# Performance work log

Hardware: AMD Instinct MI355X
Metric: run time of the kernel (lower is better)

The kernel has to match this reference:

```python
import jax, jax.numpy as jnp
import numpy as np

B, T, I, H, D, C, OUT = 32, 128, 64, 256, 32, 64, 32
DECAY = 0.99

def _lin(k, fi, fo):
    lim = 1.0 / np.sqrt(fi)
    kw, kb = jax.random.split(k)
    W = jax.random.uniform(kw, (fi, fo), minval=-lim, maxval=lim, dtype=jnp.float32)
    b = jax.random.uniform(kb, (fo,), minval=-lim, maxval=lim, dtype=jnp.float32)
    return W, b

def setup_inputs():
    key = jax.random.key(0)
    ks = jax.random.split(key, 12)
    x = jax.random.normal(ks[0], (B, T, I), dtype=jnp.float32)
    lengths = jax.random.randint(ks[1], (B,), 1, T + 1)
    W_dg1, b_dg1 = _lin(ks[2], I + H, D)
    W_dg2, b_dg2 = _lin(ks[3], D, D)
    W_e1, b_e1 = _lin(ks[4], 2 * I, H)
    W_e2, b_e2 = _lin(ks[5], H, H)
    W_ih, b_ih = _lin(ks[6], H, 3 * H)
    W_hh, b_hh = _lin(ks[7], H, 3 * H)
    W_f1, b_f1 = _lin(ks[8], H, H)
    W_f2, b_f2 = _lin(ks[9], H, C)
    return dict(x=x, lengths=lengths, out_lengths=OUT,
                W_dg1=W_dg1, b_dg1=b_dg1, W_dg2=W_dg2, b_dg2=b_dg2,
                W_e1=W_e1, b_e1=b_e1, W_e2=W_e2, b_e2=b_e2,
                W_ih=W_ih, b_ih=b_ih, W_hh=W_hh, b_hh=b_hh,
                W_f1=W_f1, b_f1=b_f1, W_f2=W_f2, b_f2=b_f2)

def _forward(x, lengths, out_lengths, W_dg1, b_dg1, W_dg2, b_dg2, W_e1, b_e1, W_e2, b_e2,
             W_ih, b_ih, W_hh, b_hh, W_f1, b_f1, W_f2, b_f2):
    Bs, Ts, Is = x.shape
    Ds = W_dg2.shape[1]
    Hs = W_e2.shape[1]
    decay = DECAY ** jnp.arange(1, Ds + 1, dtype=x.dtype)  # [D]
    d_idx = jnp.arange(Ds)
    gkey = jax.random.key(42)
    g_enc = jax.random.gumbel(jax.random.fold_in(gkey, 0), (Ts, Bs, Ds), x.dtype)
    g_dec = jax.random.gumbel(jax.random.fold_in(gkey, 1), (out_lengths, Bs, Ds), x.dtype)
    masks = (jnp.arange(Ts)[None, :] < lengths[:, None]).astype(x.dtype)  # [B,T]

    def gumbel_softmax_hard(logits, g):
        # F.gumbel_softmax(..., tau=1.0, hard=True) straight-through estimator
        y_soft = jax.nn.softmax(logits + g, axis=-1)
        y_hard = jax.nn.one_hot(jnp.argmax(y_soft, axis=-1), Ds, dtype=logits.dtype)
        return y_hard + y_soft - jax.lax.stop_gradient(y_soft)

    def gru_cell(xin, h):
        # torch.nn.GRUCell gate order: r, z, n
        gi = xin @ W_ih + b_ih
        gh = h @ W_hh + b_hh
        i_r, i_z, i_n = jnp.split(gi, 3, axis=-1)
        h_r, h_z, h_n = jnp.split(gh, 3, axis=-1)
        r = jax.nn.sigmoid(i_r + h_r)
        z = jax.nn.sigmoid(i_z + h_z)
        n = jnp.tanh(i_n + r * h_n)
        return (1.0 - z) * n + z * h

    def step_core(buf, h, x_t, g_t, mem_t):
        cell_in = jnp.concatenate([x_t, h], axis=-1)
        logits = jax.nn.elu(cell_in @ W_dg1 + b_dg1) @ W_dg2 + b_dg2
        gate = gumbel_softmax_hard(logits, g_t)  # [B,D]
        # shift buffer along dim 1 (new[:, :-1] = old[:, 1:], last slot zeroed)
        new_buf = jnp.concatenate([buf[:, 1:], jnp.zeros_like(buf[:, :1])], axis=1)
        upd = x_t[:, None, :] * decay[None, :, None] * gate[:, :, None]  # [B,D,I]
        new_buf = new_buf.at[:, d_idx, d_idx].set(upd)  # diagonal scatter-assign
        rnn_in = jnp.concatenate([x_t, mem_t], axis=-1)
        rnn_in = jax.nn.elu(rnn_in @ W_e1 + b_e1) @ W_e2 + b_e2
        return new_buf, gru_cell(rnn_in, h)

    buf0 = jnp.zeros((Bs, Ds + 1, Ds, Is), x.dtype)
    h0 = jnp.zeros((Bs, Hs), x.dtype)

    def enc_step(carry, inp):
        buf, h = carry
        x_t, m_t, g_t = inp
        mem_t = buf[:, 0].sum(axis=1)  # [B,I]
        buf, nh = step_core(buf, h, x_t, g_t, mem_t)
        h = m_t[:, None] * nh + (1.0 - m_t[:, None]) * h
        return (buf, h), None

    (buf, h), _ = jax.lax.scan(enc_step, (buf0, h0),
                               (jnp.swapaxes(x, 0, 1), masks.T, g_enc))

    x_zero = jnp.zeros((Bs, Is), x.dtype)

    def dec_step(carry, g_t):
        buf, h = carry
        # get_current_memory(slide=True): roll -1 along dim1 with last slot zeroed
        buf = jnp.concatenate([buf[:, 1:], jnp.zeros_like(buf[:, :1])], axis=1)
        mem_t = buf[:, 0].sum(axis=1)
        buf, nh = step_core(buf, h, x_zero, g_t, mem_t)
        out = jax.nn.relu(nh @ W_f1 + b_f1) @ W_f2 + b_f2
        return (buf, nh), out

    _, outs = jax.lax.scan(dec_step, (buf, h), g_dec)  # [OUT,B,C]
    return jnp.swapaxes(outs, 0, 1)  # [B,OUT,C]

def reference(x, lengths, out_lengths, W_dg1, b_dg1, W_dg2, b_dg2, W_e1, b_e1, W_e2, b_e2,
              W_ih, b_ih, W_hh, b_hh, W_f1, b_f1, W_f2, b_f2):
    return _forward(x, lengths, out_lengths, W_dg1, b_dg1, W_dg2, b_dg2, W_e1, b_e1,
                    W_e2, b_e2, W_ih, b_ih, W_hh, b_hh, W_f1, b_f1, W_f2, b_f2)
```

## Files before the change

kernel.cpp:

```cpp
#include <hip/hip_runtime.h>
#include <math.h>


#define kB 32
#define kT 128
#define kI 64
#define kH 256
#define kD 32
#define kC 64
#define kOut 32
#define kSteps (kT + kOut)
#define NB 89
#define NTHR 256
#define NT_ALL (NB * NTHR)

#define WS_FL    384
#define WS_H     1856
#define WS_SEL   (WS_H + 4*8192)
#define WS_MEM   (WS_SEL + 128)
#define WS_NZ    (WS_MEM + kB*kSteps*kI)
#define WS_LIN   WS_NZ
#define WS_O1    (WS_LIN + 4*8192)
#define WS_W2    (WS_O1 + 4*8192)
#define WS_B2    (WS_W2 + kH*3*kH)
#define WS_G     (WS_B2 + 3*kH)
#define WS_P     (WS_G + kT*kB*kD)
#define WS_ZERO_BYTES ((size_t)WS_NZ * sizeof(float))

__device__ __forceinline__ float cload(const float* p) {
  return __hip_atomic_load(p, __ATOMIC_RELAXED, __HIP_MEMORY_SCOPE_AGENT);
}
__device__ __forceinline__ void cstore(float* p, float v) {
  __hip_atomic_store(p, v, __ATOMIC_RELAXED, __HIP_MEMORY_SCOPE_AGENT);
}
__device__ __forceinline__ int cload_i(const int* p) {
  return __hip_atomic_load(p, __ATOMIC_RELAXED, __HIP_MEMORY_SCOPE_AGENT);
}
__device__ __forceinline__ void cstore_i(int* p, int v) {
  __hip_atomic_store(p, v, __ATOMIC_RELAXED, __HIP_MEMORY_SCOPE_AGENT);
}
__device__ __forceinline__ float4 cload4(const float* p) {
  float4 r;
  asm volatile("global_load_dwordx4 %0, %1, off sc0 sc1" : "=v"(r) : "v"(p));
  return r;
}
__device__ __forceinline__ void waitvm() {
  asm volatile("s_waitcnt vmcnt(0)" ::: "memory");
}

__device__ __forceinline__ void poll(const int* FL, int tid,
                                     int tH, int tDG, int tE, int tF1, int tF2) {
  int thr;
  if      (tid < 32) thr = tH;
  else if (tid == 32) thr = tDG;
  else if (tid < 65) thr = tE;
  else if (tid < 81) thr = tF1;
  else if (tid < 89) thr = tF2;
  else thr = 0;
  const int* p = FL + tid * 16;
  for (;;) {
    int ok = (thr <= 0) || (cload_i(p) >= thr);
    if (__syncthreads_count(ok) == NTHR) return;
    __builtin_amdgcn_s_sleep(2);
  }
}
__device__ __forceinline__ void setflag(int* FL, int tid, int idx, int val) {
  waitvm();
  __syncthreads();
  if (tid == 0) cstore_i(FL + idx * 16, val);
}

__device__ __forceinline__ void tf2x32(unsigned k0, unsigned k1,
                                       unsigned x0, unsigned x1,
                                       unsigned& o0, unsigned& o1) {
  unsigned ks2 = k0 ^ k1 ^ 0x1BD11BDAu;
  unsigned v0 = x0 + k0, v1 = x1 + k1;
#define TFR(r) { v0 += v1; v1 = (v1 << (r)) | (v1 >> (32-(r))); v1 ^= v0; }
  TFR(13) TFR(15) TFR(26) TFR(6)   v0 += k1;  v1 += ks2 + 1u;
  TFR(17) TFR(29) TFR(16) TFR(24)  v0 += ks2; v1 += k0  + 2u;
  TFR(13) TFR(15) TFR(26) TFR(6)   v0 += k0;  v1 += k1  + 3u;
  TFR(17) TFR(29) TFR(16) TFR(24)  v0 += k1;  v1 += ks2 + 4u;
  TFR(13) TFR(15) TFR(26) TFR(6)   v0 += ks2; v1 += k0  + 5u;
#undef TFR
  o0 = v0; o1 = v1;
}
__device__ __forceinline__ float bits_to_gumbel(unsigned bits) {
  float f = __uint_as_float((bits >> 9) | 0x3F800000u) - 1.0f;
  float u = f + 1.17549435e-38f;
  return -logf(-logf(u));
}

__device__ __forceinline__ void gridbar_full(unsigned* u, unsigned target) {
  __syncthreads();
  if (threadIdx.x == 0) {
    __threadfence();
    __hip_atomic_fetch_add(&u[320], 1u, __ATOMIC_ACQ_REL, __HIP_MEMORY_SCOPE_AGENT);
    while (__hip_atomic_load(&u[320], __ATOMIC_RELAXED, __HIP_MEMORY_SCOPE_AGENT) < target)
      __builtin_amdgcn_s_sleep(1);
    __threadfence();
  }
  __syncthreads();
}

__device__ __forceinline__ float elu1(float v) { return v > 0.f ? v : expm1f(v); }

__global__ __launch_bounds__(NTHR)
void delay_rnn(const float* __restrict__ x, const int* __restrict__ lengths,
               const float* __restrict__ W_dg1, const float* __restrict__ b_dg1,
               const float* __restrict__ W_dg2, const float* __restrict__ b_dg2,
               const float* __restrict__ W_e1,  const float* __restrict__ b_e1,
               const float* __restrict__ W_e2,  const float* __restrict__ b_e2,
               const float* __restrict__ W_ih,  const float* __restrict__ b_ih,
               const float* __restrict__ W_hh,  const float* __restrict__ b_hh,
               const float* __restrict__ W_f1,  const float* __restrict__ b_f1,
               const float* __restrict__ W_f2,  const float* __restrict__ b_f2,
               float* __restrict__ out, float* __restrict__ ws) {
  const int tid = threadIdx.x;
  const int bid = blockIdx.x;
  const int gid = bid * NTHR + tid;

  unsigned* baru = (unsigned*)ws;
  int*   FL    = (int*)(ws + WS_FL);
  float* hBuf  = ws + WS_H;
  int*   selG  = (int*)(ws + WS_SEL);
  float* mem   = ws + WS_MEM;
  float* linB  = ws + WS_LIN;
  float* o1B   = ws + WS_O1;
  float* W2g   = ws + WS_W2;
  float* B2g   = ws + WS_B2;
  float* g     = ws + WS_G;
  float* Pg    = ws + WS_P;

  __shared__ float S[35264];
  __shared__ float lgarr[1056];
  __shared__ float sb1[32], sb2[32], dec_sh[32];
  __shared__ int   sel[32], len_s[32];

  {
    unsigned k0, k1;
    tf2x32(0u, 42u, 0u, 0u, k0, k1);
    for (int i = gid; i < kT * kB * kD; i += NT_ALL) {
      unsigned a, b;
      tf2x32(k0, k1, 0u, (unsigned)i, a, b);
      g[i] = bits_to_gumbel(a ^ b);
    }
  }
  for (int idx = gid; idx < kH * 3 * kH; idx += NT_ALL) {
    int k = idx / (3 * kH), n = idx % (3 * kH);
    const float* wr = W_e2 + k * kH;
    float s0 = 0, s1 = 0, s2 = 0, s3 = 0;
    for (int m = 0; m < kH; m += 4) {
      float4 wv = *(const float4*)(wr + m);
      s0 += wv.x * W_ih[(m    ) * 3 * kH + n];
      s1 += wv.y * W_ih[(m + 1) * 3 * kH + n];
      s2 += wv.z * W_ih[(m + 2) * 3 * kH + n];
      s3 += wv.w * W_ih[(m + 3) * 3 * kH + n];
    }
    W2g[idx] = ((s0 + s1) + (s2 + s3));
  }
  for (int n = gid; n < 3 * kH; n += NT_ALL) {
    float s = b_ih[n];
    for (int m = 0; m < kH; ++m) s += b_e2[m] * W_ih[m * 3 * kH + n];
    B2g[n] = s;
  }
  for (int idx = gid; idx < kT * kB * kH; idx += NT_ALL) {
    int s = idx >> 13, r = idx & 8191, b = r >> 8, j = r & 255;
    const float* xr = x + (b * kT + s) * kI;
    float a0 = 0, a1 = 0, a2 = 0, a3 = 0;
    for (int k = 0; k < 64; k += 4) {
      float4 xv = *(const float4*)(xr + k);
      a0 += xv.x * W_e1[(64 + k) * 256 + j];
      a1 += xv.y * W_e1[(65 + k) * 256 + j];
      a2 += xv.z * W_e1[(66 + k) * 256 + j];
      a3 += xv.w * W_e1[(67 + k) * 256 + j];
    }
    Pg[idx] = ((a0 + a1) + (a2 + a3));
  }

  gridbar_full(baru, NB);

  if (bid < 32) {
    float* whh = S; float* w2 = S + 6240;
    const int jb = bid * 8;
    for (int i = tid; i < 6144; i += NTHR) {
      int gg = i >> 11, r = i & 2047, jj = r >> 8, k = r & 255;
      whh[(gg * 8 + jj) * 260 + k] = W_hh[k * 768 + gg * 256 + jb + jj];
      w2 [(gg * 8 + jj) * 260 + k] = W2g [k * 768 + gg * 256 + jb + jj];
    }
    if (tid < 24) { int gg = tid / 8, jj = tid % 8;
      sb1[tid] = b_hh[gg * 256 + jb + jj];
      sb2[tid] = B2g [gg * 256 + jb + jj];
    }
    if (tid < 32) len_s[tid] = lengths[tid];
    __syncthreads();

    float* sH = S + 12480; float* sLin = S + 20800;
    float* red = S + 29120;
    for (int s = 0; s < kSteps; ++s) {
      int tDG = (s >= 1) ? (s < kT ? s : kT) : 0;
      int tF1 = (s >= kT + 4) ? (s - 2) : 0;
      poll(FL, tid, s, tDG, s + 1, tF1, 0);

      const float* hR = hBuf + (s & 3) * 8192;
      const float* lR = linB + (s & 3) * 8192;
      const bool useC = (s >= 1 && s < kT);
      const float4* P4 = (const float4*)(Pg + (s - 1) * 8192);
      const int* selR = selG + ((s - 1) & 3) * 32;
      float4 th[8], tl[8], tp[8];
      int tsel[8];
      #pragma unroll
      for (int u8 = 0; u8 < 8; ++u8) {
        int i4 = (tid + u8 * 256) * 4;
        th[u8] = cload4(hR + i4);
        tl[u8] = cload4(lR + i4);
      }
      if (useC) {
        #pragma unroll
        for (int u8 = 0; u8 < 8; ++u8) {
          int idx = tid + u8 * 256; int b = idx >> 6, k4 = idx & 63;
          tp[u8] = P4[b * 64 + k4];
          tsel[u8] = cload_i(&selR[b]);
        }
      }
      waitvm();
      #pragma unroll
      for (int u8 = 0; u8 < 8; ++u8) {
        int idx = tid + u8 * 256; int b = idx >> 6, k4 = idx & 63;
        *(float4*)&sH[b * 260 + k4 * 4] = th[u8];
        float cx = 0.f, cy = 0.f, cz = 0.f, cw = 0.f;
        if (useC && tsel[u8] == 0) {
          cx = 0.99f * tp[u8].x; cy = 0.99f * tp[u8].y;
          cz = 0.99f * tp[u8].z; cw = 0.99f * tp[u8].w;
        }
        float4 v;
        v.x = elu1(tl[u8].x + cx);
        v.y = elu1(tl[u8].y + cy);
        v.z = elu1(tl[u8].z + cz);
        v.w = elu1(tl[u8].w + cw);
        *(float4*)&sLin[b * 260 + k4 * 4] = v;
      }
      __syncthreads();
      const float4* sH4 = (const float4*)sH;
      const float4* sL4 = (const float4*)sLin;
      const float4* wh4 = (const float4*)whh;
      const float4* w24 = (const float4*)w2;
      const int c  = tid & 7;
      const int b4 = (tid >> 3) & 7;
      const int kq = tid >> 6;
      float acc[24];
      #pragma unroll
      for (int a = 0; a < 24; ++a) acc[a] = 0.f;
      for (int kk = 0; kk < 16; ++kk) {
        int k4 = kq * 16 + kk;
        float4 wr[6];
        #pragma unroll
        for (int gg = 0; gg < 3; ++gg) {
          wr[gg]     = wh4[(gg * 8 + c) * 65 + k4];
          wr[3 + gg] = w24[(gg * 8 + c) * 65 + k4];
        }
        #pragma unroll
        for (int bi = 0; bi < 4; ++bi) {
          int b = bi * 8 + b4;
          float4 h4 = sH4[b * 65 + k4];
          float4 l4 = sL4[b * 65 + k4];
          #pragma unroll
          for (int gg = 0; gg < 3; ++gg) {
            float4 w = wr[gg];
            acc[bi * 6 + gg]     += h4.x * w.x + h4.y * w.y + h4.z * w.z + h4.w * w.w;
            w = wr[3 + gg];
            acc[bi * 6 + 3 + gg] += l4.x * w.x + l4.y * w.y + l4.z * w.z + l4.w * w.w;
          }
        }
      }
      #pragma unroll
      for (int bi = 0; bi < 4; ++bi)
        #pragma unroll
        for (int rr = 0; rr < 6; ++rr)
          red[kq * 1536 + rr * 256 + (bi * 8 + b4) * 8 + c] = acc[bi * 6 + rr];
      __syncthreads();
      {
        int b = tid >> 3, cc = tid & 7, jg = bid * 8 + cc;
        int lo = b * 8 + cc;
        float dots[6];
        #pragma unroll
        for (int rr = 0; rr < 6; ++rr)
          dots[rr] = (red[rr * 256 + lo] + red[1536 + rr * 256 + lo]) +
                     (red[3072 + rr * 256 + lo] + red[4608 + rr * 256 + lo]);
        float ghr = dots[0] + sb1[cc];
        float ghz = dots[1] + sb1[8 + cc];
        float ghn = dots[2] + sb1[16 + cc];
        float gir = dots[3] + sb2[cc];
        float giz = dots[4] + sb2[8 + cc];
        float gin = dots[5] + sb2[16 + cc];
        float r = 1.f / (1.f + expf(-(gir + ghr)));
        float z = 1.f / (1.f + expf(-(giz + ghz)));
        float n = tanhf(gin + r * ghn);
        float hold = sH[b * 260 + jg];
        float nh = (1.f - z) * n + z * hold;
        float hv = (s < kT) ? ((s < len_s[b]) ? nh : hold) : nh;
        cstore(&hBuf[((s + 1) & 3) * 8192 + b * 256 + jg], hv);
      }
      setflag(FL, tid, bid, s + 1);
    }
  }
  else if (bid < 64) {
    float* we1 = S;
    const int jb = (bid - 32) * 8;
    for (int i = tid; i < 1024; i += NTHR) {
      int jj = i >> 7, k = i & 127;
      we1[jj * 132 + k] = W_e1[k * 256 + jb + jj];
    }
    if (tid < 8) sb1[tid] = b_e1[jb + tid];
    __syncthreads();

    float* sx = S + 1056; float* sm = S + 3232;
    for (int e = 0; e < kSteps; ++e) {
      int tDG = e - 1 < 0 ? 0 : (e - 1 > kT ? kT : e - 1);
      poll(FL, tid, e - 2, tDG, 0, 0, 0);

      const bool encx = (e < kT);
      float4 tm[2];
      #pragma unroll
      for (int u2 = 0; u2 < 2; ++u2) {
        int idx = tid + u2 * 256; int b = idx >> 4, k4 = idx & 15;
        tm[u2] = cload4(mem + (b * kSteps + e) * kI + k4 * 4);
      }
      waitvm();
      #pragma unroll
      for (int u2 = 0; u2 < 2; ++u2) {
        int idx = tid + u2 * 256; int b = idx >> 4, k4 = idx & 15;
        *(float4*)&sm[b * 68 + k4 * 4] = tm[u2];
        if (encx)
          *(float4*)&sx[b * 68 + k4 * 4] =
              *(const float4*)(x + (b * kT + e) * kI + k4 * 4);
      }
      __syncthreads();
      const int b = tid >> 3, jj = tid & 7;
      const float4* sx4 = (const float4*)sx;
      const float4* sm4 = (const float4*)sm;
      const float4* w4p = (const float4*)we1;
      float a0 = 0, a1 = 0, a2 = 0, a3 = 0;
      if (encx) {
        for (int k4 = 0; k4 < 16; ++k4) {
          float4 xv = sx4[b * 17 + k4], w = w4p[jj * 33 + k4];
          a0 += xv.x * w.x; a1 += xv.y * w.y; a2 += xv.z * w.z; a3 += xv.w * w.w;
        }
      }
      for (int k4 = 0; k4 < 16; ++k4) {
        float4 mv = sm4[b * 17 + k4], w = w4p[jj * 33 + 16 + k4];
        a0 += mv.x * w.x; a1 += mv.y * w.y; a2 += mv.z * w.z; a3 += mv.w * w.w;
      }
      cstore(&linB[(e & 3) * 8192 + b * 256 + jb + jj],
             ((a0 + a1) + (a2 + a3)) + sb1[jj]);
      __syncthreads();
      setflag(FL, tid, 33 + (bid - 32), e + 1);
    }
  }
  else if (bid < 80) {
    float* wf1 = S;
    const int jb = (bid - 64) * 16;
    for (int i = tid; i < 4096; i += NTHR) {
      int jj = i >> 8, k = i & 255;
      wf1[jj * 260 + k] = W_f1[k * 256 + jb + jj];
    }
    if (tid < 16) sb1[tid] = b_f1[jb + tid];
    __syncthreads();

    float* sHf = S + 4160; float* red = S + 12480;
    for (int s = kT + 1; s <= kSteps; ++s) {
      int tF2 = (s >= kT + 5) ? (s - 2) : 0;
      poll(FL, tid, s, 0, 0, 0, tF2);

      const float* hR = hBuf + (s & 3) * 8192;
      float4 th[8];
      #pragma unroll
      for (int u8 = 0; u8 < 8; ++u8) th[u8] = cload4(hR + (tid + u8 * 256) * 4);
      waitvm();
      #pragma unroll
      for (int u8 = 0; u8 < 8; ++u8) {
        int idx = tid + u8 * 256; int b = idx >> 6, k4 = idx & 63;
        *(float4*)&sHf[b * 260 + k4 * 4] = th[u8];
      }
      __syncthreads();
      const float4* sH4 = (const float4*)sHf;
      const float4* w4p = (const float4*)wf1;
      const int cq = tid & 3, b4 = (tid >> 2) & 7, kq = tid >> 5;
      float acc[16];
      #pragma unroll
      for (int a = 0; a < 16; ++a) acc[a] = 0.f;
      for (int kk = 0; kk < 8; ++kk) {
        int k4 = kq * 8 + kk;
        float4 wr[4];
        #pragma unroll
        for (int ci = 0; ci < 4; ++ci) wr[ci] = w4p[(cq * 4 + ci) * 65 + k4];
        #pragma unroll
        for (int bi = 0; bi < 4; ++bi) {
          float4 h4 = sH4[(bi * 8 + b4) * 65 + k4];
          #pragma unroll
          for (int ci = 0; ci < 4; ++ci) {
            float4 w = wr[ci];
            acc[bi * 4 + ci] += h4.x * w.x + h4.y * w.y + h4.z * w.z + h4.w * w.w;
          }
        }
      }
      #pragma unroll
      for (int bi = 0; bi < 4; ++bi)
        #pragma unroll
        for (int ci = 0; ci < 4; ++ci)
          red[kq * 512 + (bi * 4 + ci) * 32 + cq * 8 + b4] = acc[bi * 4 + ci];
      __syncthreads();
      #pragma unroll
      for (int u2 = 0; u2 < 2; ++u2) {
        int o = tid * 2 + u2; int b = o >> 4, col = o & 15;
        int gg = ((b >> 3) * 4 + (col & 3)) * 32 + (col >> 2) * 8 + (b & 7);
        float v = 0.f;
        #pragma unroll
        for (int kq2 = 0; kq2 < 8; ++kq2) v += red[kq2 * 512 + gg];
        v += sb1[col];
        cstore(&o1B[(s & 3) * 8192 + b * 256 + (bid - 64) * 16 + col],
               v > 0.f ? v : 0.f);
      }
      __syncthreads();
      setflag(FL, tid, 65 + (bid - 64), s + 1);
    }
  }
  else if (bid < 88) {
    float* wf2 = S;
    const int cb = (bid - 80) * 8;
    for (int i = tid; i < 2048; i += NTHR) {
      int cc = i >> 8, k = i & 255;
      wf2[cc * 260 + k] = W_f2[k * 64 + cb + cc];
    }
    if (tid < 8) sb2[tid] = b_f2[cb + tid];
    __syncthreads();

    float* sO = S + 2080; float* red = S + 10400;
    for (int s = kT + 2; s <= kSteps + 1; ++s) {
      poll(FL, tid, 0, 0, 0, s, 0);

      const float* oR = o1B + ((s - 1) & 3) * 8192;
      float4 to[8];
      #pragma unroll
      for (int u8 = 0; u8 < 8; ++u8) to[u8] = cload4(oR + (tid + u8 * 256) * 4);
      waitvm();
      #pragma unroll
      for (int u8 = 0; u8 < 8; ++u8) {
        int idx = tid + u8 * 256; int b = idx >> 6, k4 = idx & 63;
        *(float4*)&sO[b * 260 + k4 * 4] = to[u8];
      }
      __syncthreads();
      const float4* sO4 = (const float4*)sO;
      const float4* w4p = (const float4*)wf2;
      const int c = tid & 7, b4 = (tid >> 3) & 7, kq = tid >> 6;
      float acc[4] = {0.f, 0.f, 0.f, 0.f};
      for (int kk = 0; kk < 16; ++kk) {
        int k4 = kq * 16 + kk;
        float4 w = w4p[c * 65 + k4];
        #pragma unroll
        for (int bi = 0; bi < 4; ++bi) {
          float4 o4 = sO4[(bi * 8 + b4) * 65 + k4];
          acc[bi] += o4.x * w.x + o4.y * w.y + o4.z * w.z + o4.w * w.w;
        }
      }
      #pragma unroll
      for (int bi = 0; bi < 4; ++bi)
        red[kq * 256 + bi * 64 + b4 * 8 + c] = acc[bi];
      __syncthreads();
      { int b = tid >> 3, col = tid & 7;
        int gg = (b >> 3) * 64 + (b & 7) * 8 + col;
        float v = (red[gg] + red[256 + gg]) + (red[512 + gg] + red[768 + gg]);
        out[(b * kOut + (s - 2 - kT)) * kC + (bid - 80) * 8 + col] =
            v + sb2[col];
      }
      __syncthreads();
      setflag(FL, tid, 81 + (bid - 80), s + 1);
    }
  }
  else {
    float* wdg1 = S; float* wdg2 = S + 10368;
    for (int i = tid; i < 10240; i += NTHR) {
      int j = i / 320, k = i % 320;
      wdg1[j * 324 + k] = W_dg1[k * 32 + j];
    }
    for (int i = tid; i < 1024; i += NTHR) wdg2[i] = W_dg2[i];
    if (tid < 32) { sb1[tid] = b_dg1[tid]; sb2[tid] = b_dg2[tid];
                    dec_sh[tid] = powf(0.99f, (float)(tid + 1)); }
    __syncthreads();

    float* sXH = S + 11392;
    float* red = S + 21760;
    float* l1s = S + 25856;
    for (int s = 0; s < kT; ++s) {
      poll(FL, tid, s, 0, 0, 0, 0);

      const float* hR = hBuf + (s & 3) * 8192;
      float4 th[8];
      #pragma unroll
      for (int u8 = 0; u8 < 8; ++u8) th[u8] = cload4(hR + (tid + u8 * 256) * 4);
      waitvm();
      #pragma unroll
      for (int u8 = 0; u8 < 8; ++u8) {
        int idx = tid + u8 * 256; int b = idx >> 6, k4 = idx & 63;
        *(float4*)&sXH[b * 324 + 64 + k4 * 4] = th[u8];
      }
      #pragma unroll
      for (int u2 = 0; u2 < 2; ++u2) {
        int idx = tid + u2 * 256; int b = idx >> 4, k4 = idx & 15;
        *(float4*)&sXH[b * 324 + k4 * 4] =
            *(const float4*)(x + (b * kT + s) * kI + k4 * 4);
      }
      __syncthreads();
      {
        const float4* sA4 = (const float4*)sXH;
        const float4* wd4 = (const float4*)wdg1;
        const int cq = tid & 7, b4 = (tid >> 3) & 7, kq = tid >> 6;
        float acc[16];
        #pragma unroll
        for (int a = 0; a < 16; ++a) acc[a] = 0.f;
        for (int kk = 0; kk < 20; ++kk) {
          int k4 = kq * 20 + kk;
          float4 wr[4];
          #pragma unroll
          for (int ci = 0; ci < 4; ++ci) wr[ci] = wd4[(cq * 4 + ci) * 81 + k4];
          #pragma unroll
          for (int bi = 0; bi < 4; ++bi) {
            float4 a4 = sA4[(bi * 8 + b4) * 81 + k4];
            #pragma unroll
            for (int ci = 0; ci < 4; ++ci) {
              float4 w = wr[ci];
              acc[bi * 4 + ci] += a4.x * w.x + a4.y * w.y + a4.z * w.z + a4.w * w.w;
            }
          }
        }
        #pragma unroll
        for (int bi = 0; bi < 4; ++bi)
          #pragma unroll
          for (int ci = 0; ci < 4; ++ci)
            red[kq * 1024 + (ci * 4 + bi) * 64 + cq * 8 + b4] = acc[bi * 4 + ci];
        __syncthreads();
        #pragma unroll
        for (int u4 = 0; u4 < 4; ++u4) {
          int o = tid * 4 + u4; int b = o >> 5, col = o & 31;
          int ci = col & 3, cq2 = col >> 2, bi = b >> 3, b42 = b & 7;
          int f = (ci * 4 + bi) * 64 + cq2 * 8 + b42;
          float v = (red[f] + red[1024 + f]) + (red[2048 + f] + red[3072 + f]);
          l1s[b * 36 + col] = elu1(v + sb1[col]);
        }
      }
      __syncthreads();
      for (int it = 0; it < 4; ++it) {
        int i = tid + it * 256; int b = i >> 5, j = i & 31;
        float sv = sb2[j];
        for (int k = 0; k < 32; ++k) sv += l1s[b * 36 + k] * wdg2[k * 32 + j];
        lgarr[b * 33 + j] = sv + g[(s * 32 + b) * 32 + j];
      }
      __syncthreads();
      if (tid < 32) {
        float best = lgarr[tid * 33]; int bi = 0;
        for (int j = 1; j < 32; ++j) {
          float v = lgarr[tid * 33 + j];
          if (v > best) { best = v; bi = j; }
        }
        sel[tid] = bi;
      }
      __syncthreads();
      if (tid < 32) cstore_i(&selG[(s & 3) * 32 + tid], sel[tid]);
      for (int it = 0; it < 8; ++it) {
        int i = tid + it * 256; int b = i >> 6, ii = i & 63;
        int d = sel[b];
        if (d > 0) {
          int c = s + 1 + d, e = -1;
          if (c < kT) e = c;
          else { int rr = c - kT - 1;
                 if (rr >= 0 && !(rr & 1)) { int kk = rr >> 1; if (kk < kOut) e = kT + kk; } }
          if (e >= 0) {
            float* p = &mem[(b * kSteps + e) * kI + ii];
            cstore(p, cload(p) + sXH[b * 324 + ii] * dec_sh[d]);
          }
        }
      }
      setflag(FL, tid, 32, s + 1);
    }
  }
}

extern "C" void kernel_launch(void* const* d_in, const int* in_sizes, int n_in,
                              void* d_out, int out_size, void* d_ws, size_t ws_size,
                              hipStream_t stream) {
  (void)in_sizes; (void)n_in; (void)out_size; (void)ws_size;
  const float* x      = (const float*)d_in[0];
  const int*   lens   = (const int*)  d_in[1];
  const float* W_dg1  = (const float*)d_in[3];
  const float* b_dg1  = (const float*)d_in[4];
  const float* W_dg2  = (const float*)d_in[5];
  const float* b_dg2  = (const float*)d_in[6];
  const float* W_e1   = (const float*)d_in[7];
  const float* b_e1   = (const float*)d_in[8];
  const float* W_e2   = (const float*)d_in[9];
  const float* b_e2   = (const float*)d_in[10];
  const float* W_ih   = (const float*)d_in[11];
  const float* b_ih   = (const float*)d_in[12];
  const float* W_hh   = (const float*)d_in[13];
  const float* b_hh   = (const float*)d_in[14];
  const float* W_f1   = (const float*)d_in[15];
  const float* b_f1   = (const float*)d_in[16];
  const float* W_f2   = (const float*)d_in[17];
  const float* b_f2   = (const float*)d_in[18];

  hipMemsetAsync(d_ws, 0, WS_ZERO_BYTES, stream);
  delay_rnn<<<dim3(NB), dim3(NTHR), 0, stream>>>(
      x, lens, W_dg1, b_dg1, W_dg2, b_dg2, W_e1, b_e1, W_e2, b_e2,
      W_ih, b_ih, W_hh, b_hh, W_f1, b_f1, W_f2, b_f2,
      (float*)d_out, (float*)d_ws);
}
```

Baseline: 1.941 ms.

## Fold encoder-linear and delay-gate blocks into GRU blocks, precompute input projection

Removes the dedicated encoder-linear blocks and the single delay-gate block. The x-part of the first encoder linear is now precomputed for all steps in the prologue. Each GRU block redundantly computes the delay-gate argmax itself and applies the delayed memory contribution straight into the precomputed linear buffer, using the already projected P rows. This cuts the grid from 89 to 56 blocks and removes two inter-block flag hops on the recurrent critical path. In exchange, every GRU block repeats the small gate matmul each step, and the prologue grows.

```diff
diff --git a/kernel.cpp b/kernel.cpp
--- a/kernel.cpp
+++ b/kernel.cpp
@@ -10,21 +10,20 @@
 #define kC 64
 #define kOut 32
 #define kSteps (kT + kOut)
-#define NB 89
+#define NB 56
 #define NTHR 256
 #define NT_ALL (NB * NTHR)
 
 #define WS_FL    384
 #define WS_H     1856
-#define WS_SEL   (WS_H + 4*8192)
-#define WS_MEM   (WS_SEL + 128)
-#define WS_NZ    (WS_MEM + kB*kSteps*kI)
-#define WS_LIN   WS_NZ
-#define WS_O1    (WS_LIN + 4*8192)
-#define WS_W2    (WS_O1 + 4*8192)
+#define WS_NZ    (WS_H + 4*8192)
+#define WS_DG1T  WS_NZ
+#define WS_W2    (WS_DG1T + 32*320)
 #define WS_B2    (WS_W2 + kH*3*kH)
 #define WS_G     (WS_B2 + 3*kH)
 #define WS_P     (WS_G + kT*kB*kD)
+#define WS_LINF  (WS_P + kT*kB*kH)
+#define WS_O1    (WS_LINF + kSteps*kB*kH)
 #define WS_ZERO_BYTES ((size_t)WS_NZ * sizeof(float))
 
 __device__ __forceinline__ float cload(const float* p) {
@@ -44,18 +43,21 @@
   asm volatile("global_load_dwordx4 %0, %1, off sc0 sc1" : "=v"(r) : "v"(p));
   return r;
 }
+__device__ __forceinline__ void cstore4(float* p, float4 v) {
+  cstore(p + 0, v.x); cstore(p + 1, v.y);
+  cstore(p + 2, v.z); cstore(p + 3, v.w);
+}
 __device__ __forceinline__ void waitvm() {
   asm volatile("s_waitcnt vmcnt(0)" ::: "memory");
 }
 
 __device__ __forceinline__ void poll(const int* FL, int tid,
-                                     int tH, int tDG, int tE, int tF1, int tF2) {
+                                     int tH, int tD, int tF1, int tF2) {
   int thr;
   if      (tid < 32) thr = tH;
-  else if (tid == 32) thr = tDG;
-  else if (tid < 65) thr = tE;
-  else if (tid < 81) thr = tF1;
-  else if (tid < 89) thr = tF2;
+  else if (tid < 64) thr = tD;
+  else if (tid < 80) thr = tF1;
+  else if (tid < 88) thr = tF2;
   else thr = 0;
   const int* p = FL + tid * 16;
   for (;;) {
@@ -122,19 +124,17 @@
   unsigned* baru = (unsigned*)ws;
   int*   FL    = (int*)(ws + WS_FL);
   float* hBuf  = ws + WS_H;
-  int*   selG  = (int*)(ws + WS_SEL);
-  float* mem   = ws + WS_MEM;
-  float* linB  = ws + WS_LIN;
-  float* o1B   = ws + WS_O1;
+  float* dg1T  = ws + WS_DG1T;
   float* W2g   = ws + WS_W2;
   float* B2g   = ws + WS_B2;
   float* g     = ws + WS_G;
   float* Pg    = ws + WS_P;
-
-  __shared__ float S[35264];
-  __shared__ float lgarr[1056];
-  __shared__ float sb1[32], sb2[32], dec_sh[32];
-  __shared__ int   sel[32], len_s[32];
+  float* linF  = ws + WS_LINF;
+  float* o1B   = ws + WS_O1;
+
+  __shared__ float S[38464];
+  __shared__ float sb1[32], sb2[32], dec_sh[32], dgb1[32], dgb2[32];
+  __shared__ int   sel_sh[32], len_s[32];
 
   {
     unsigned k0, k1;
@@ -144,6 +144,10 @@
       tf2x32(k0, k1, 0u, (unsigned)i, a, b);
       g[i] = bits_to_gumbel(a ^ b);
     }
+  }
+  for (int i = gid; i < 32 * 320; i += NT_ALL) {
+    int j = i / 320, k = i % 320;
+    dg1T[i] = W_dg1[k * 32 + j];
   }
   for (int idx = gid; idx < kH * 3 * kH; idx += NT_ALL) {
     int k = idx / (3 * kH), n = idx % (3 * kH);
@@ -176,61 +180,76 @@
     }
     Pg[idx] = ((a0 + a1) + (a2 + a3));
   }
+  for (int idx = gid; idx < kSteps * kB * kH; idx += NT_ALL) {
+    int e = idx >> 13, r = idx & 8191, b = r >> 8, j = r & 255;
+    float v = b_e1[j];
+    if (e < kT) {
+      const float* xr = x + (b * kT + e) * kI;
+      float a0 = 0, a1 = 0, a2 = 0, a3 = 0;
+      for (int k = 0; k < 64; k += 4) {
+        float4 xv = *(const float4*)(xr + k);
+        a0 += xv.x * W_e1[(k    ) * 256 + j];
+        a1 += xv.y * W_e1[(k + 1) * 256 + j];
+        a2 += xv.z * W_e1[(k + 2) * 256 + j];
+        a3 += xv.w * W_e1[(k + 3) * 256 + j];
+      }
+      v += ((a0 + a1) + (a2 + a3));
+    }
+    linF[idx] = v;
+  }
 
   gridbar_full(baru, NB);
 
   if (bid < 32) {
     float* whh = S; float* w2 = S + 6240;
+    float* sH = S + 12480; float* sLin = S + 20800;
+    float* red = S + 29120;
+    float* sX = S + 35264;
+    float* wdg2 = S + 37440;
     const int jb = bid * 8;
     for (int i = tid; i < 6144; i += NTHR) {
       int gg = i >> 11, r = i & 2047, jj = r >> 8, k = r & 255;
       whh[(gg * 8 + jj) * 260 + k] = W_hh[k * 768 + gg * 256 + jb + jj];
       w2 [(gg * 8 + jj) * 260 + k] = W2g [k * 768 + gg * 256 + jb + jj];
     }
+    for (int i = tid; i < 1024; i += NTHR) wdg2[i] = W_dg2[i];
     if (tid < 24) { int gg = tid / 8, jj = tid % 8;
       sb1[tid] = b_hh[gg * 256 + jb + jj];
       sb2[tid] = B2g [gg * 256 + jb + jj];
     }
-    if (tid < 32) len_s[tid] = lengths[tid];
+    if (tid < 32) {
+      len_s[tid] = lengths[tid];
+      dgb1[tid] = b_dg1[tid]; dgb2[tid] = b_dg2[tid];
+      dec_sh[tid] = powf(0.99f, (float)(tid + 1));
+    }
     __syncthreads();
 
-    float* sH = S + 12480; float* sLin = S + 20800;
-    float* red = S + 29120;
     for (int s = 0; s < kSteps; ++s) {
-      int tDG = (s >= 1) ? (s < kT ? s : kT) : 0;
+      int tD  = (s >= 2) ? ((s < kT) ? (s - 1) : kT) : 0;
       int tF1 = (s >= kT + 4) ? (s - 2) : 0;
-      poll(FL, tid, s, tDG, s + 1, tF1, 0);
+      poll(FL, tid, s, tD, tF1, 0);
 
       const float* hR = hBuf + (s & 3) * 8192;
-      const float* lR = linB + (s & 3) * 8192;
+      const float* lR = linF + s * 8192;
       const bool useC = (s >= 1 && s < kT);
       const float4* P4 = (const float4*)(Pg + (s - 1) * 8192);
-      const int* selR = selG + ((s - 1) & 3) * 32;
-      float4 th[8], tl[8], tp[8];
-      int tsel[8];
+      float4 th[8], tl[8];
       #pragma unroll
       for (int u8 = 0; u8 < 8; ++u8) {
         int i4 = (tid + u8 * 256) * 4;
         th[u8] = cload4(hR + i4);
         tl[u8] = cload4(lR + i4);
       }
-      if (useC) {
-        #pragma unroll
-        for (int u8 = 0; u8 < 8; ++u8) {
-          int idx = tid + u8 * 256; int b = idx >> 6, k4 = idx & 63;
-          tp[u8] = P4[b * 64 + k4];
-          tsel[u8] = cload_i(&selR[b]);
-        }
-      }
       waitvm();
       #pragma unroll
       for (int u8 = 0; u8 < 8; ++u8) {
         int idx = tid + u8 * 256; int b = idx >> 6, k4 = idx & 63;
         *(float4*)&sH[b * 260 + k4 * 4] = th[u8];
         float cx = 0.f, cy = 0.f, cz = 0.f, cw = 0.f;
-        if (useC && tsel[u8] == 0) {
-          cx = 0.99f * tp[u8].x; cy = 0.99f * tp[u8].y;
-          cz = 0.99f * tp[u8].z; cw = 0.99f * tp[u8].w;
+        if (useC && sel_sh[b] == 0) {
+          float4 p = P4[b * 64 + k4];
+          cx = 0.99f * p.x; cy = 0.99f * p.y;
+          cz = 0.99f * p.z; cw = 0.99f * p.w;
         }
         float4 v;
         v.x = elu1(tl[u8].x + cx);
@@ -301,64 +320,102 @@
         cstore(&hBuf[((s + 1) & 3) * 8192 + b * 256 + jg], hv);
       }
       setflag(FL, tid, bid, s + 1);
-    }
-  }
-  else if (bid < 64) {
-    float* we1 = S;
-    const int jb = (bid - 32) * 8;
-    for (int i = tid; i < 1024; i += NTHR) {
-      int jj = i >> 7, k = i & 127;
-      we1[jj * 132 + k] = W_e1[k * 256 + jb + jj];
-    }
-    if (tid < 8) sb1[tid] = b_e1[jb + tid];
-    __syncthreads();
-
-    float* sx = S + 1056; float* sm = S + 3232;
-    for (int e = 0; e < kSteps; ++e) {
-      int tDG = e - 1 < 0 ? 0 : (e - 1 > kT ? kT : e - 1);
-      poll(FL, tid, e - 2, tDG, 0, 0, 0);
-
-      const bool encx = (e < kT);
-      float4 tm[2];
-      #pragma unroll
-      for (int u2 = 0; u2 < 2; ++u2) {
-        int idx = tid + u2 * 256; int b = idx >> 4, k4 = idx & 15;
-        tm[u2] = cload4(mem + (b * kSteps + e) * kI + k4 * 4);
-      }
-      waitvm();
-      #pragma unroll
-      for (int u2 = 0; u2 < 2; ++u2) {
-        int idx = tid + u2 * 256; int b = idx >> 4, k4 = idx & 15;
-        *(float4*)&sm[b * 68 + k4 * 4] = tm[u2];
-        if (encx)
-          *(float4*)&sx[b * 68 + k4 * 4] =
-              *(const float4*)(x + (b * kT + e) * kI + k4 * 4);
-      }
-      __syncthreads();
-      const int b = tid >> 3, jj = tid & 7;
-      const float4* sx4 = (const float4*)sx;
-      const float4* sm4 = (const float4*)sm;
-      const float4* w4p = (const float4*)we1;
-      float a0 = 0, a1 = 0, a2 = 0, a3 = 0;
-      if (encx) {
-        for (int k4 = 0; k4 < 16; ++k4) {
-          float4 xv = sx4[b * 17 + k4], w = w4p[jj * 33 + k4];
-          a0 += xv.x * w.x; a1 += xv.y * w.y; a2 += xv.z * w.z; a3 += xv.w * w.w;
-        }
-      }
-      for (int k4 = 0; k4 < 16; ++k4) {
-        float4 mv = sm4[b * 17 + k4], w = w4p[jj * 33 + 16 + k4];
-        a0 += mv.x * w.x; a1 += mv.y * w.y; a2 += mv.z * w.z; a3 += mv.w * w.w;
-      }
-      cstore(&linB[(e & 3) * 8192 + b * 256 + jb + jj],
-             ((a0 + a1) + (a2 + a3)) + sb1[jj]);
-      __syncthreads();
-      setflag(FL, tid, 33 + (bid - 32), e + 1);
-    }
-  }
-  else if (bid < 80) {
+
+      if (s < kT) {
+        #pragma unroll
+        for (int u2 = 0; u2 < 2; ++u2) {
+          int idx = tid + u2 * 256; int b = idx >> 4, k4 = idx & 15;
+          *(float4*)&sX[b * 68 + k4 * 4] =
+              *(const float4*)(x + (b * kT + s) * kI + k4 * 4);
+        }
+        __syncthreads();
+        {
+          const float4* sX4 = (const float4*)sX;
+          const float4* sHq = (const float4*)sH;
+          const float4* wd4 = (const float4*)dg1T;
+          const int cq = tid & 7, b42 = (tid >> 3) & 7, kq2 = tid >> 6;
+          float acc2[16];
+          #pragma unroll
+          for (int a = 0; a < 16; ++a) acc2[a] = 0.f;
+          for (int kk = 0; kk < 20; ++kk) {
+            int k4 = kq2 * 20 + kk;
+            float4 wr[4];
+            #pragma unroll
+            for (int ci = 0; ci < 4; ++ci) wr[ci] = wd4[(cq * 4 + ci) * 80 + k4];
+            const bool isx = (k4 < 16);
+            #pragma unroll
+            for (int bi = 0; bi < 4; ++bi) {
+              int b = bi * 8 + b42;
+              float4 a4 = isx ? sX4[b * 17 + k4] : sHq[b * 65 + (k4 - 16)];
+              #pragma unroll
+              for (int ci = 0; ci < 4; ++ci) {
+                float4 w = wr[ci];
+                acc2[bi * 4 + ci] += a4.x * w.x + a4.y * w.y + a4.z * w.z + a4.w * w.w;
+              }
+            }
+          }
+          #pragma unroll
+          for (int bi = 0; bi < 4; ++bi)
+            #pragma unroll
+            for (int ci = 0; ci < 4; ++ci)
+              red[kq2 * 1024 + (ci * 4 + bi) * 64 + cq * 8 + b42] = acc2[bi * 4 + ci];
+        }
+        __syncthreads();
+        float* l1s = red + 4096;
+        #pragma unroll
+        for (int u4 = 0; u4 < 4; ++u4) {
+          int o = tid * 4 + u4; int b = o >> 5, col = o & 31;
+          int ci = col & 3, cq2 = col >> 2, bi = b >> 3, b42 = b & 7;
+          int f = (ci * 4 + bi) * 64 + cq2 * 8 + b42;
+          float v = (red[f] + red[1024 + f]) + (red[2048 + f] + red[3072 + f]);
+          l1s[b * 36 + col] = elu1(v + dgb1[col]);
+        }
+        __syncthreads();
+        float* lg = red;
+        for (int it = 0; it < 4; ++it) {
+          int i = tid + it * 256; int b = i >> 5, j = i & 31;
+          float sv = dgb2[j];
+          for (int k = 0; k < 32; ++k) sv += l1s[b * 36 + k] * wdg2[k * 32 + j];
+          lg[b * 33 + j] = sv + g[(s * 32 + b) * 32 + j];
+        }
+        __syncthreads();
+        if (tid < 32) {
+          float best = lg[tid * 33]; int bj = 0;
+          for (int j = 1; j < 32; ++j) {
+            float v = lg[tid * 33 + j];
+            if (v > best) { best = v; bj = j; }
+          }
+          sel_sh[tid] = bj;
+        }
+        __syncthreads();
+        {
+          int d = sel_sh[bid];
+          if (d > 0) {
+            int cc = s + 1 + d, e = -1;
+            if (cc < kT) e = cc;
+            else { int rr = cc - kT - 1;
+                   if (rr >= 0 && !(rr & 1)) {
+                     int kk2 = rr >> 1; if (kk2 < kOut) e = kT + kk2; } }
+            if (e >= 0 && tid < 64) {
+              float dec = dec_sh[d];
+              float* rowp = linF + e * 8192 + bid * 256;
+              const float* Prow = Pg + s * 8192 + bid * 256;
+              float4 v = cload4(rowp + tid * 4);
+              float4 p = *(const float4*)(Prow + tid * 4);
+              waitvm();
+              v.x += dec * p.x; v.y += dec * p.y;
+              v.z += dec * p.z; v.w += dec * p.w;
+              cstore4(rowp + tid * 4, v);
+            }
+          }
+        }
+        setflag(FL, tid, 32 + bid, s + 1);
+      }
+    }
+  }
+  else if (bid < 48) {
     float* wf1 = S;
-    const int jb = (bid - 64) * 16;
+    const int jb = (bid - 32) * 16;
     for (int i = tid; i < 4096; i += NTHR) {
       int jj = i >> 8, k = i & 255;
       wf1[jj * 260 + k] = W_f1[k * 256 + jb + jj];
@@ -369,7 +426,7 @@
     float* sHf = S + 4160; float* red = S + 12480;
     for (int s = kT + 1; s <= kSteps; ++s) {
       int tF2 = (s >= kT + 5) ? (s - 2) : 0;
-      poll(FL, tid, s, 0, 0, 0, tF2);
+      poll(FL, tid, s, 0, 0, tF2);
 
       const float* hR = hBuf + (s & 3) * 8192;
       float4 th[8];
@@ -417,16 +474,16 @@
         #pragma unroll
         for (int kq2 = 0; kq2 < 8; ++kq2) v += red[kq2 * 512 + gg];
         v += sb1[col];
-        cstore(&o1B[(s & 3) * 8192 + b * 256 + (bid - 64) * 16 + col],
+        cstore(&o1B[(s & 3) * 8192 + b * 256 + (bid - 32) * 16 + col],
                v > 0.f ? v : 0.f);
       }
       __syncthreads();
-      setflag(FL, tid, 65 + (bid - 64), s + 1);
-    }
-  }
-  else if (bid < 88) {
+      setflag(FL, tid, 64 + (bid - 32), s + 1);
+    }
+  }
+  else {
     float* wf2 = S;
-    const int cb = (bid - 80) * 8;
+    const int cb = (bid - 48) * 8;
     for (int i = tid; i < 2048; i += NTHR) {
       int cc = i >> 8, k = i & 255;
       wf2[cc * 260 + k] = W_f2[k * 64 + cb + cc];
@@ -436,7 +493,7 @@
 
     float* sO = S + 2080; float* red = S + 10400;
     for (int s = kT + 2; s <= kSteps + 1; ++s) {
-      poll(FL, tid, 0, 0, 0, s, 0);
+      poll(FL, tid, 0, 0, s, 0);
 
       const float* oR = o1B + ((s - 1) & 3) * 8192;
       float4 to[8];
@@ -469,117 +526,11 @@
       { int b = tid >> 3, col = tid & 7;
         int gg = (b >> 3) * 64 + (b & 7) * 8 + col;
         float v = (red[gg] + red[256 + gg]) + (red[512 + gg] + red[768 + gg]);
-        out[(b * kOut + (s - 2 - kT)) * kC + (bid - 80) * 8 + col] =
+        out[(b * kOut + (s - 2 - kT)) * kC + (bid - 48) * 8 + col] =
             v + sb2[col];
       }
       __syncthreads();
-      setflag(FL, tid, 81 + (bid - 80), s + 1);
-    }
-  }
-  else {
-    float* wdg1 = S; float* wdg2 = S + 10368;
-    for (int i = tid; i < 10240; i += NTHR) {
-      int j = i / 320, k = i % 320;
-      wdg1[j * 324 + k] = W_dg1[k * 32 + j];
-    }
-    for (int i = tid; i < 1024; i += NTHR) wdg2[i] = W_dg2[i];
-    if (tid < 32) { sb1[tid] = b_dg1[tid]; sb2[tid] = b_dg2[tid];
-                    dec_sh[tid] = powf(0.99f, (float)(tid + 1)); }
-    __syncthreads();
-
-    float* sXH = S + 11392;
-    float* red = S + 21760;
-    float* l1s = S + 25856;
-    for (int s = 0; s < kT; ++s) {
-      poll(FL, tid, s, 0, 0, 0, 0);
-
-      const float* hR = hBuf + (s & 3) * 8192;
-      float4 th[8];
-      #pragma unroll
-      for (int u8 = 0; u8 < 8; ++u8) th[u8] = cload4(hR + (tid + u8 * 256) * 4);
-      waitvm();
-      #pragma unroll
-      for (int u8 = 0; u8 < 8; ++u8) {
-        int idx = tid + u8 * 256; int b = idx >> 6, k4 = idx & 63;
-        *(float4*)&sXH[b * 324 + 64 + k4 * 4] = th[u8];
-      }
-      #pragma unroll
-      for (int u2 = 0; u2 < 2; ++u2) {
-        int idx = tid + u2 * 256; int b = idx >> 4, k4 = idx & 15;
-        *(float4*)&sXH[b * 324 + k4 * 4] =
-            *(const float4*)(x + (b * kT + s) * kI + k4 * 4);
-      }
-      __syncthreads();
-      {
-        const float4* sA4 = (const float4*)sXH;
-        const float4* wd4 = (const float4*)wdg1;
-        const int cq = tid & 7, b4 = (tid >> 3) & 7, kq = tid >> 6;
-        float acc[16];
-        #pragma unroll
-        for (int a = 0; a < 16; ++a) acc[a] = 0.f;
-        for (int kk = 0; kk < 20; ++kk) {
-          int k4 = kq * 20 + kk;
-          float4 wr[4];
-          #pragma unroll
-          for (int ci = 0; ci < 4; ++ci) wr[ci] = wd4[(cq * 4 + ci) * 81 + k4];
-          #pragma unroll
-          for (int bi = 0; bi < 4; ++bi) {
-            float4 a4 = sA4[(bi * 8 + b4) * 81 + k4];
-            #pragma unroll
-            for (int ci = 0; ci < 4; ++ci) {
-              float4 w = wr[ci];
-              acc[bi * 4 + ci] += a4.x * w.x + a4.y * w.y + a4.z * w.z + a4.w * w.w;
-            }
-          }
-        }
-        #pragma unroll
-        for (int bi = 0; bi < 4; ++bi)
-          #pragma unroll
-          for (int ci = 0; ci < 4; ++ci)
-            red[kq * 1024 + (ci * 4 + bi) * 64 + cq * 8 + b4] = acc[bi * 4 + ci];
-        __syncthreads();
-        #pragma unroll
-        for (int u4 = 0; u4 < 4; ++u4) {
-          int o = tid * 4 + u4; int b = o >> 5, col = o & 31;
-          int ci = col & 3, cq2 = col >> 2, bi = b >> 3, b42 = b & 7;
-          int f = (ci * 4 + bi) * 64 + cq2 * 8 + b42;
-          float v = (red[f] + red[1024 + f]) + (red[2048 + f] + red[3072 + f]);
-          l1s[b * 36 + col] = elu1(v + sb1[col]);
-        }
-      }
-      __syncthreads();
-      for (int it = 0; it < 4; ++it) {
-        int i = tid + it * 256; int b = i >> 5, j = i & 31;
-        float sv = sb2[j];
-        for (int k = 0; k < 32; ++k) sv += l1s[b * 36 + k] * wdg2[k * 32 + j];
-        lgarr[b * 33 + j] = sv + g[(s * 32 + b) * 32 + j];
-      }
-      __syncthreads();
-      if (tid < 32) {
-        float best = lgarr[tid * 33]; int bi = 0;
-        for (int j = 1; j < 32; ++j) {
-          float v = lgarr[tid * 33 + j];
-          if (v > best) { best = v; bi = j; }
-        }
-        sel[tid] = bi;
-      }
-      __syncthreads();
-      if (tid < 32) cstore_i(&selG[(s & 3) * 32 + tid], sel[tid]);
-      for (int it = 0; it < 8; ++it) {
-        int i = tid + it * 256; int b = i >> 6, ii = i & 63;
-        int d = sel[b];
-        if (d > 0) {
-          int c = s + 1 + d, e = -1;
-          if (c < kT) e = c;
-          else { int rr = c - kT - 1;
-                 if (rr >= 0 && !(rr & 1)) { int kk = rr >> 1; if (kk < kOut) e = kT + kk; } }
-          if (e >= 0) {
-            float* p = &mem[(b * kSteps + e) * kI + ii];
-            cstore(p, cload(p) + sXH[b * 324 + ii] * dec_sh[d]);
-          }
-        }
-      }
-      setflag(FL, tid, 32, s + 1);
+      setflag(FL, tid, 80 + (bid - 48), s + 1);
     }
   }
 }
```

New measurement: 3.569 ms. 1.84x slower.
